# Kernel optimization log

Measured on AMD Instinct MI355X. Metric: run time of the kernel, lower is better.

Reference implementation:

```python
import jax, jax.numpy as jnp
import numpy as np

D_MODEL, D_STATE, D_CONV, EXPAND, L = 512, 16, 4, 2, 2048
D_INNER = EXPAND * D_MODEL


def _dwconv_causal(x, w, b):
    # x: (L, D), w: (D, K), b: (D,). torch Conv1d(groups=D, padding=K-1)[..., :L]
    K = w.shape[1]
    xp = jnp.pad(x, ((K - 1, 0), (0, 0)))
    windows = jnp.stack([xp[k:k + x.shape[0]] for k in range(K)], axis=-1)  # (L, D, K)
    return jnp.einsum('ldk,dk->ld', windows, w) + b


def _ssm_dir(x, inW, inb, cw, cb, xpW, xpb, dtW, dtb, outW, outb, A_log, Dp):
    xz = x @ inW + inb                      # (L, 2*Di)
    x_ssm, z = xz[:, :D_INNER], xz[:, D_INNER:]
    x_ssm = _dwconv_causal(x_ssm, cw, cb)   # (L, Di)
    sp = jax.nn.silu(x_ssm) @ xpW + xpb     # (L, Di + 2*S)
    delta = sp[:, :D_INNER]
    B = sp[:, D_INNER:D_INNER + D_STATE]
    C = sp[:, D_INNER + D_STATE:]
    dt = jax.nn.softplus(delta @ dtW + dtb)  # (L, Di)
    A = -jnp.exp(A_log)                      # (Di, S)
    dA = jnp.exp(dt[:, :, None] * A[None])                      # (L, Di, S)
    dBu = dt[:, :, None] * B[:, None, :] * x_ssm[:, :, None]    # (L, Di, S)

    def step(h, inp):
        a, bu = inp
        h = a * h + bu
        return h, h

    h0 = jnp.zeros((D_INNER, D_STATE), x.dtype)
    _, hs = jax.lax.scan(step, h0, (dA, dBu))   # (L, Di, S)
    y = jnp.einsum('lds,ls->ld', hs, C) + Dp * x_ssm
    return (y * jax.nn.silu(z)) @ outW + outb


def _make_params(key):
    ks = jax.random.split(key, 32)
    i = iter(range(32))
    def w(shape, scale=0.02):
        return (jax.random.normal(ks[next(i)], shape, jnp.float32) * scale)
    p = {}
    for pre in ('fwd_', 'bwd_'):
        p[pre + 'in_W'] = w((D_MODEL, 2 * D_INNER))
        p[pre + 'in_b'] = w((2 * D_INNER,))
        p[pre + 'conv_w'] = w((D_INNER, D_CONV), 0.1)
        p[pre + 'conv_b'] = w((D_INNER,))
        p[pre + 'xp_W'] = w((D_INNER, D_INNER + 2 * D_STATE))
        p[pre + 'xp_b'] = w((D_INNER + 2 * D_STATE,))
        p[pre + 'dt_W'] = w((D_INNER, D_INNER))
        p[pre + 'dt_b'] = w((D_INNER,))
        p[pre + 'out_W'] = w((D_INNER, D_MODEL))
        p[pre + 'out_b'] = w((D_MODEL,))
    p['A_log'] = jax.random.normal(ks[next(i)], (D_INNER, D_STATE), jnp.float32) * 0.5
    p['D_param'] = jnp.ones((D_INNER,), jnp.float32)
    p['fusion_W'] = w((2 * D_MODEL, D_MODEL))
    p['fusion_b'] = w((D_MODEL,))
    return p


def setup_inputs() -> dict:
    key = jax.random.key(0)
    kx, kp = jax.random.split(key)
    inp = {'x': jax.random.normal(kx, (L, D_MODEL), jnp.float32)}
    inp.update(_make_params(kp))
    return inp


def reference(x,
              fwd_in_W, fwd_in_b, fwd_conv_w, fwd_conv_b, fwd_xp_W, fwd_xp_b,
              fwd_dt_W, fwd_dt_b, fwd_out_W, fwd_out_b,
              bwd_in_W, bwd_in_b, bwd_conv_w, bwd_conv_b, bwd_xp_W, bwd_xp_b,
              bwd_dt_W, bwd_dt_b, bwd_out_W, bwd_out_b,
              A_log, D_param, fusion_W, fusion_b):
    out_fwd = _ssm_dir(x, fwd_in_W, fwd_in_b, fwd_conv_w, fwd_conv_b,
                       fwd_xp_W, fwd_xp_b, fwd_dt_W, fwd_dt_b,
                       fwd_out_W, fwd_out_b, A_log, D_param)
    out_bwd = _ssm_dir(x[::-1], bwd_in_W, bwd_in_b, bwd_conv_w, bwd_conv_b,
                       bwd_xp_W, bwd_xp_b, bwd_dt_W, bwd_dt_b,
                       bwd_out_W, bwd_out_b, A_log, D_param)[::-1]
    return jnp.concatenate([out_fwd, out_bwd], axis=-1) @ fusion_W + fusion_b
```

## Files before the change

kernel.cpp:

```cpp
#include <hip/hip_runtime.h>
#include <cmath>

#define L_SEQ 2048
#define DM 512
#define DI 1024
#define DS 16
#define NSP 1056
#define NC 64
#define CL 32

typedef unsigned short ushortT;
typedef unsigned int u32;
typedef __attribute__((ext_vector_type(8))) short short8;
typedef __attribute__((ext_vector_type(4))) unsigned short ushort4_t;
typedef __attribute__((ext_vector_type(4))) float float4_t;
typedef __attribute__((address_space(1))) u32 gu32;
typedef __attribute__((address_space(3))) u32 lu32;

__device__ __forceinline__ float sigm(float x) { return 1.0f / (1.0f + __expf(-x)); }

__device__ __forceinline__ ushortT f2bf(float f) {
    unsigned u = __float_as_uint(f);
    unsigned r = u + 0x7FFFu + ((u >> 16) & 1u);
    return (ushortT)(r >> 16);
}
__device__ __forceinline__ float b2f(ushortT u) {
    return __uint_as_float(((u32)u) << 16);
}
__device__ __forceinline__ void gl2lds16(const ushortT* g, ushortT* l) {
    __builtin_amdgcn_global_load_lds((gu32*)g, (lu32*)l, 16, 0, 0);
}

struct WC {
    const float* src[11];
    ushortT* dst[11];
    int ss[11], soff[11], ds_[11], tN[11], mode[11];
    int off[12];
};

struct KP {
    WC wc; int nW, nprep;
    const float* x; ushortT* XB;
    const float *xpb0, *xpb1, *dtW0, *dtW1, *dtb0, *dtb1;
    const float *outb0, *outb1, *fuW, *fub;
    float *BFdt0, *BFdt1, *BFof;
    const float *inb0, *inb1;
    ushortT *WtIn, *WtDt, *WtFu, *WtXpF, *XpD, *OutC, *WtOF2;
    ushortT *XSb, *Zb, *SCb, *DTbB, *Gb;
    float *BCf;
    const float *cw0, *cw1, *cb0, *cb1;
    const float *Alog, *Dp;
    float *Pend, *Hl, *Hs;
    float* out;
};

template<int BM, int BN>
__device__ void gemm_core(
    ushortT* As, ushortT* Bs, int bm, int bn,
    const ushortT* __restrict__ A, int lda, int revA,
    const ushortT* __restrict__ A2, int dualK,
    const ushortT* __restrict__ W,
    const float* __restrict__ bias,
    float* __restrict__ Cf, int ldcf,
    float* __restrict__ Cf2, int ldcf2, int Nsplit,
    ushortT* __restrict__ Cb, int ldcb,
    ushortT* __restrict__ Cb2, int ldcb2,
    int M, int N, int K, int epi)
{
    constexpr int BK = 64;
    constexpr int MI = BM / 32;
    constexpr int NI = BN / 32;
    constexpr int CA = BM / 32;
    constexpr int CB = BN / 32;

    const int tid  = threadIdx.x;
    const int wave = tid >> 6;
    const int lane = tid & 63;
    const int quad = lane >> 4;
    const int r    = lane & 15;
    const int wm   = (wave >> 1) * (BM / 2);
    const int wn   = (wave & 1) * (BN / 2);

    const int lrow = lane >> 3;
    const int lk   = ((lane & 7) ^ lrow) * 8;

    const ushortT* gA[CA]; const ushortT* gA2[CA]; ushortT* lA[CA];
    #pragma unroll
    for (int c = 0; c < CA; ++c) {
        int row = bm + c * 32 + wave * 8 + lrow;
        int r0 = revA ? (M - 1 - row) : row;
        gA[c] = A + (size_t)r0 * lda + lk;
        gA2[c] = dualK ? (A2 + (size_t)(M - 1 - row) * lda + lk) : gA[c];
        lA[c] = &As[(c * 32 + wave * 8) * BK];
    }
    const ushortT* gB[CB]; ushortT* lB[CB];
    #pragma unroll
    for (int c = 0; c < CB; ++c) {
        int row = bn + c * 32 + wave * 8 + lrow;
        if (row > N - 1) row = N - 1;
        gB[c] = W + (size_t)row * K + lk;
        lB[c] = &Bs[(c * 32 + wave * 8) * BK];
    }

    float4_t acc[MI][NI];
    #pragma unroll
    for (int i = 0; i < MI; ++i)
        #pragma unroll
        for (int j = 0; j < NI; ++j)
            acc[i][j] = (float4_t){0.f, 0.f, 0.f, 0.f};

    const int nsteps = K >> 6;

    auto stage = [&](int step) {
        int kq = step << 6;
        #pragma unroll
        for (int c = 0; c < CA; ++c) {
            const ushortT* s = (!dualK || kq < 1024) ? gA[c] + kq : gA2[c] + (kq - 1024);
            gl2lds16(s, lA[c]);
        }
        #pragma unroll
        for (int c = 0; c < CB; ++c)
            gl2lds16(gB[c] + kq, lB[c]);
    };
    auto compute = [&]() {
        #pragma unroll
        for (int kh = 0; kh < 2; ++kh) {
            const int slot = (((kh * 4 + quad) ^ (lane & 7)) * 8);
            short8 af[MI], bf[NI];
            #pragma unroll
            for (int mi = 0; mi < MI; ++mi)
                af[mi] = *(const short8*)&As[(wm + mi * 16 + r) * BK + slot];
            #pragma unroll
            for (int ni = 0; ni < NI; ++ni)
                bf[ni] = *(const short8*)&Bs[(wn + ni * 16 + r) * BK + slot];
            #pragma unroll
            for (int mi = 0; mi < MI; ++mi)
                #pragma unroll
                for (int ni = 0; ni < NI; ++ni)
                    acc[mi][ni] = __builtin_amdgcn_mfma_f32_16x16x32_bf16(
                        af[mi], bf[ni], acc[mi][ni], 0, 0, 0);
        }
    };

    stage(0);
    for (int i = 0; i < nsteps; ++i) {
        __syncthreads();
        compute();
        if (i + 1 < nsteps) {
            __syncthreads();
            stage(i + 1);
        }
    }

    #pragma unroll
    for (int mi = 0; mi < MI; ++mi) {
        int rowb = bm + wm + mi * 16 + quad * 4;
        #pragma unroll
        for (int ni = 0; ni < NI; ++ni) {
            int gn = bn + wn + ni * 16 + r;
            if (gn < N) {
                float bv = bias ? bias[gn] : 0.0f;
                #pragma unroll
                for (int j = 0; j < 4; ++j) {
                    int orow = rowb + j;
                    float v = acc[mi][ni][j] + bv;
                    if (gn < Nsplit) {
                        if (epi == 1) v = (v > 20.0f) ? v : log1pf(__expf(v));
                        if (Cf) Cf[(size_t)orow * ldcf + gn] = v;
                        if (Cb) Cb[(size_t)orow * ldcb + gn] = f2bf(v);
                    } else {
                        if (Cf2) Cf2[(size_t)orow * ldcf2 + gn - Nsplit] = v;
                        if (Cb2) Cb2[(size_t)orow * ldcb2 + gn - Nsplit] = f2bf(v);
                    }
                }
            }
        }
    }
}

__global__ __launch_bounds__(256) void prep_k(KP p)
{
    __shared__ ushortT smem[2624];
    ushortT (*t)[33] = (ushortT(*)[33])smem;
    float* red = (float*)(smem + 2112);
    int b = blockIdx.x;
    int tid = threadIdx.x;
    if (b < p.nW) {
        const WC& wc = p.wc;
        int m = 0;
        while (b >= wc.off[m + 1]) ++m;
        int tl = b - wc.off[m];
        int n0 = (tl % wc.tN[m]) * 32;
        int k0 = (tl / wc.tN[m]) * 32;
        const float* W = wc.src[m];
        ushortT* D = wc.dst[m];
        int ss = wc.ss[m], soff = wc.soff[m], ds = wc.ds_[m];
        int tx = tid & 31, ty = tid >> 5;
        if (wc.mode[m] == 1) {
            #pragma unroll
            for (int i = 0; i < 32; i += 8)
                D[(size_t)(k0 + ty + i) * ds + n0 + tx] =
                    f2bf(W[(size_t)(k0 + ty + i) * ss + soff + n0 + tx]);
        } else {
            #pragma unroll
            for (int i = 0; i < 32; i += 8)
                t[ty + i][tx] = f2bf(W[(size_t)(k0 + ty + i) * ss + soff + n0 + tx]);
            __syncthreads();
            #pragma unroll
            for (int i = 0; i < 32; i += 8)
                D[(size_t)(n0 + ty + i) * ds + k0 + tx] = t[tx][ty + i];
        }
        return;
    }
    b -= p.nW;
    if (b < 1024) {
        int i = (b * 256 + tid) * 4;
        float4_t v = *(const float4_t*)(p.x + i);
        p.XB[i + 0] = f2bf(v[0]); p.XB[i + 1] = f2bf(v[1]);
        p.XB[i + 2] = f2bf(v[2]); p.XB[i + 3] = f2bf(v[3]);
        return;
    }
    int o = b - 1024;
    float acc = 0.0f;
    if (o < 2112) {
        int dir = o >= 1056;
        int m = o - dir * 1056;
        const float* xpb = dir ? p.xpb1 : p.xpb0;
        float* BF = dir ? p.BFdt1 : p.BFdt0;
        if (m >= 1024) {
            if (tid == 0) BF[m] = xpb[m];
            return;
        }
        const float* dtW = dir ? p.dtW1 : p.dtW0;
        const float* dtb = dir ? p.dtb1 : p.dtb0;
        for (int n = tid; n < 1024; n += 256) acc += xpb[n] * dtW[n * 1024 + m];
        red[tid] = acc;
        __syncthreads();
        for (int s = 128; s > 0; s >>= 1) {
            if (tid < s) red[tid] += red[tid + s];
            __syncthreads();
        }
        if (tid == 0) BF[m] = red[0] + dtb[m];
    } else {
        int n = o - 2112;
        for (int j = tid; j < 1024; j += 256) {
            float ob = (j < 512) ? p.outb0[j] : p.outb1[j - 512];
            acc += ob * p.fuW[(size_t)j * 512 + n];
        }
        red[tid] = acc;
        __syncthreads();
        for (int s = 128; s > 0; s >>= 1) {
            if (tid < s) red[tid] += red[tid + s];
            __syncthreads();
        }
        if (tid == 0) p.BFof[n] = red[0] + p.fub[n];
    }
}

__global__ __launch_bounds__(256) void mega_k(KP p)
{
    __shared__ ushortT As[128 * 64];
    __shared__ ushortT Bs[64 * 64];
    int job = blockIdx.x;
    if (job < 1024) {
        int xc = job & 7;
        int k = job >> 3;
        int dir = xc & 1;
        int q = xc >> 1;
        int bx = q * 8 + (k & 7);
        int by = k >> 3;
        gemm_core<128, 64>(As, Bs, by * 128, bx * 64,
            p.XB, DM, dir, nullptr, 0,
            p.WtIn + (size_t)dir * 2 * DI * DM,
            dir ? p.inb1 : p.inb0,
            nullptr, 0, nullptr, 0, DI,
            p.XSb + (size_t)dir * L_SEQ * DI, DI,
            p.Zb + (size_t)dir * L_SEQ * DI, DI,
            L_SEQ, 2 * DI, DM, 0);
    } else if (job < 1536) {
        int j = job - 1024;
        int d = j >> 8;
        int t = j & 255;
        gemm_core<64, 64>(As, Bs, (t >> 4) * 64, (t & 15) * 64,
            p.WtDt + (size_t)d * DI * DI, DI, 0, nullptr, 0,
            p.XpD + (size_t)d * DI * DI,
            nullptr, nullptr, 0, nullptr, 0, DI,
            p.WtXpF + (size_t)d * NSP * DI, DI, nullptr, 0,
            DI, DI, DI, 0);
    } else {
        int j = job - 1536;
        int d = j >> 7;
        int t = j & 127;
        gemm_core<64, 64>(As, Bs, (t >> 4) * 64, (t & 15) * 64,
            p.WtFu + (size_t)d * DM, DI, 0, nullptr, 0,
            p.OutC + (size_t)d * DI * DM,
            nullptr, nullptr, 0, nullptr, 0, DI,
            p.WtOF2 + (size_t)d * DI, 2 * DI, nullptr, 0,
            DM, DI, DM, 0);
    }
}

__global__ __launch_bounds__(256) void conv_k(KP p)
{
    int job = blockIdx.x;
    int dir = job >> 11;
    int bx = job & 2047;
    const ushortT* XSb = p.XSb + (size_t)dir * L_SEQ * DI;
    ushortT* SCb = p.SCb + (size_t)dir * L_SEQ * DI;
    const float* cw = dir ? p.cw1 : p.cw0;
    const float* cb = dir ? p.cb1 : p.cb0;
    int idx = (bx * 256 + threadIdx.x) * 4;
    int d4 = idx & (DI - 1);
    int l = idx >> 10;
    ushort4_t r0 = *(const ushort4_t*)(XSb + (size_t)l * DI + d4);
    ushort4_t r1 = (l >= 1) ? *(const ushort4_t*)(XSb + (size_t)(l - 1) * DI + d4) : (ushort4_t){0,0,0,0};
    ushort4_t r2 = (l >= 2) ? *(const ushort4_t*)(XSb + (size_t)(l - 2) * DI + d4) : (ushort4_t){0,0,0,0};
    ushort4_t r3 = (l >= 3) ? *(const ushort4_t*)(XSb + (size_t)(l - 3) * DI + d4) : (ushort4_t){0,0,0,0};
    ushort4_t outv;
    #pragma unroll
    for (int j = 0; j < 4; ++j) {
        int d = d4 + j;
        float acc = cb[d] + cw[d * 4 + 0] * b2f(r3[j]) + cw[d * 4 + 1] * b2f(r2[j])
                  + cw[d * 4 + 2] * b2f(r1[j]) + cw[d * 4 + 3] * b2f(r0[j]);
        outv[j] = f2bf(acc * sigm(acc));
    }
    *(ushort4_t*)(SCb + idx) = outv;
}

__global__ __launch_bounds__(256) void xp_k(KP p)
{
    __shared__ ushortT As[128 * 64];
    __shared__ ushortT Bs[64 * 64];
    int job = blockIdx.x;
    int xc = job & 7;
    int k = job >> 3;
    int dir = xc & 1;
    int mq = xc >> 1;
    int bx = k >> 2;
    int by = mq * 4 + (k & 3);
    gemm_core<128, 64>(As, Bs, by * 128, bx * 64,
        p.SCb + (size_t)dir * L_SEQ * DI, DI, 0, nullptr, 0,
        p.WtXpF + (size_t)dir * NSP * DI,
        dir ? p.BFdt1 : p.BFdt0,
        nullptr, 0,
        p.BCf + (size_t)dir * L_SEQ * 32, 32, DI,
        p.DTbB + (size_t)dir * L_SEQ * DI, DI, nullptr, 0,
        L_SEQ, NSP, DI, 1);
}

__global__ __launch_bounds__(256) void scanA_k(KP p)
{
    __shared__ float Bsh[CL][DS];
    int job = blockIdx.x;
    int dir = job >> 8;
    int c = (job & 255) >> 2;
    int d = (job & 3) * 256 + threadIdx.x;
    const ushortT* DTb = p.DTbB + (size_t)dir * L_SEQ * DI;
    const ushortT* XSb = p.XSb + (size_t)dir * L_SEQ * DI;
    const float* BC = p.BCf + (size_t)dir * L_SEQ * 32;
    const float* cw = dir ? p.cw1 : p.cw0;
    const float* cb = dir ? p.cb1 : p.cb0;
    int l0 = c * CL;
    for (int i = threadIdx.x; i < CL * DS; i += 256) {
        int ll = i >> 4, ss = i & 15;
        Bsh[ll][ss] = BC[(size_t)(l0 + ll) * 32 + ss];
    }
    __syncthreads();
    float w0 = cw[d * 4 + 0], w1 = cw[d * 4 + 1], w2 = cw[d * 4 + 2], w3 = cw[d * 4 + 3];
    float cbv = cb[d];
    float x3 = (l0 >= 3) ? b2f(XSb[(size_t)(l0 - 3) * DI + d]) : 0.f;
    float x2 = (l0 >= 2) ? b2f(XSb[(size_t)(l0 - 2) * DI + d]) : 0.f;
    float x1 = (l0 >= 1) ? b2f(XSb[(size_t)(l0 - 1) * DI + d]) : 0.f;
    float Ae[DS], h[DS], P[DS];
    #pragma unroll
    for (int s = 0; s < DS; ++s) { Ae[s] = -__expf(p.Alog[d * DS + s]); h[s] = 0.f; P[s] = 1.f; }
    for (int t = 0; t < CL; ++t) {
        int l = l0 + t;
        float x0 = b2f(XSb[(size_t)l * DI + d]);
        float xv = cbv + w0 * x3 + w1 * x2 + w2 * x1 + w3 * x0;
        x3 = x2; x2 = x1; x1 = x0;
        float dt = b2f(DTb[(size_t)l * DI + d]);
        float dtx = dt * xv;
        #pragma unroll
        for (int s = 0; s < DS; ++s) {
            float e = __expf(dt * Ae[s]);
            h[s] = e * h[s] + dtx * Bsh[t][s];
            P[s] *= e;
        }
    }
    size_t o = ((size_t)(dir * NC + c) * DI + d) * DS;
    #pragma unroll
    for (int s = 0; s < DS; ++s) { p.Pend[o + s] = P[s]; p.Hl[o + s] = h[s]; }
}

__global__ __launch_bounds__(256) void scanB_k(KP p)
{
    int idx = blockIdx.x * 256 + threadIdx.x;
    float h = 0.f;
    int ds = idx & 16383;
    int dir = idx >> 14;
    for (int c = 0; c < NC; ++c) {
        size_t o = ((size_t)(dir * NC + c)) * (DI * DS) + ds;
        p.Hs[o] = h;
        h = p.Pend[o] * h + p.Hl[o];
    }
}

__global__ __launch_bounds__(256) void scanC_k(KP p)
{
    __shared__ float Bsh[CL][DS];
    __shared__ float Csh[CL][DS];
    int job = blockIdx.x;
    int dir = job >> 8;
    int c = (job & 255) >> 2;
    int d = (job & 3) * 256 + threadIdx.x;
    const ushortT* DTb = p.DTbB + (size_t)dir * L_SEQ * DI;
    const ushortT* XSb = p.XSb + (size_t)dir * L_SEQ * DI;
    const float* BC = p.BCf + (size_t)dir * L_SEQ * 32;
    const ushortT* Zb = p.Zb + (size_t)dir * L_SEQ * DI;
    ushortT* Gb = p.Gb + (size_t)dir * L_SEQ * DI;
    const float* cw = dir ? p.cw1 : p.cw0;
    const float* cb = dir ? p.cb1 : p.cb0;
    int l0 = c * CL;
    for (int i = threadIdx.x; i < CL * DS; i += 256) {
        int ll = i >> 4, ss = i & 15;
        size_t base = (size_t)(l0 + ll) * 32;
        Bsh[ll][ss] = BC[base + ss];
        Csh[ll][ss] = BC[base + DS + ss];
    }
    __syncthreads();
    float w0 = cw[d * 4 + 0], w1 = cw[d * 4 + 1], w2 = cw[d * 4 + 2], w3 = cw[d * 4 + 3];
    float cbv = cb[d];
    float x3 = (l0 >= 3) ? b2f(XSb[(size_t)(l0 - 3) * DI + d]) : 0.f;
    float x2 = (l0 >= 2) ? b2f(XSb[(size_t)(l0 - 2) * DI + d]) : 0.f;
    float x1 = (l0 >= 1) ? b2f(XSb[(size_t)(l0 - 1) * DI + d]) : 0.f;
    float Ae[DS], h[DS];
    size_t o = ((size_t)(dir * NC + c) * DI + d) * DS;
    #pragma unroll
    for (int s = 0; s < DS; ++s) { Ae[s] = -__expf(p.Alog[d * DS + s]); h[s] = p.Hs[o + s]; }
    float dpv = p.Dp[d];
    for (int t = 0; t < CL; ++t) {
        int l = l0 + t;
        float x0 = b2f(XSb[(size_t)l * DI + d]);
        float xv = cbv + w0 * x3 + w1 * x2 + w2 * x1 + w3 * x0;
        x3 = x2; x2 = x1; x1 = x0;
        float dt = b2f(DTb[(size_t)l * DI + d]);
        float dtx = dt * xv;
        float y = 0.f;
        #pragma unroll
        for (int s = 0; s < DS; ++s) {
            float e = __expf(dt * Ae[s]);
            h[s] = e * h[s] + dtx * Bsh[t][s];
            y += h[s] * Csh[t][s];
        }
        y += dpv * xv;
        float z = b2f(Zb[(size_t)l * DI + d]);
        Gb[(size_t)l * DI + d] = f2bf(y * (z * sigm(z)));
    }
}

__global__ __launch_bounds__(256) void final_k(KP p)
{
    __shared__ ushortT As[64 * 64];
    __shared__ ushortT Bs[32 * 64];
    int job = blockIdx.x;
    int xc = job & 7;
    int k = job >> 3;
    int by = xc * 4 + (k & 3);
    int bx = k >> 2;
    gemm_core<64, 32>(As, Bs, by * 64, bx * 32,
        p.Gb, DI, 0, p.Gb + (size_t)L_SEQ * DI, 1,
        p.WtOF2, p.BFof,
        p.out, DM, nullptr, 0, DM,
        nullptr, 0, nullptr, 0,
        L_SEQ, DM, 2 * DI, 0);
}

extern "C" void kernel_launch(void* const* d_in, const int* in_sizes, int n_in,
                              void* d_out, int out_size, void* d_ws, size_t ws_size,
                              hipStream_t stream)
{
    (void)in_sizes; (void)n_in; (void)out_size; (void)ws_size;
    const float* x = (const float*)d_in[0];
    const float* inW[2]  = {(const float*)d_in[1],  (const float*)d_in[11]};
    const float* inb[2]  = {(const float*)d_in[2],  (const float*)d_in[12]};
    const float* cw[2]   = {(const float*)d_in[3],  (const float*)d_in[13]};
    const float* cb[2]   = {(const float*)d_in[4],  (const float*)d_in[14]};
    const float* xpW[2]  = {(const float*)d_in[5],  (const float*)d_in[15]};
    const float* xpb[2]  = {(const float*)d_in[6],  (const float*)d_in[16]};
    const float* dtW[2]  = {(const float*)d_in[7],  (const float*)d_in[17]};
    const float* dtb[2]  = {(const float*)d_in[8],  (const float*)d_in[18]};
    const float* outW[2] = {(const float*)d_in[9],  (const float*)d_in[19]};
    const float* outb[2] = {(const float*)d_in[10], (const float*)d_in[20]};
    const float* Alog = (const float*)d_in[21];
    const float* Dp   = (const float*)d_in[22];
    const float* fuW  = (const float*)d_in[23];
    const float* fub  = (const float*)d_in[24];
    float* out = (float*)d_out;

    float* ws = (float*)d_ws;
    size_t off = 0;
    auto alloc = [&](size_t n) { float* p = ws + off; off += n; return p; };
    float* BCf  = alloc((size_t)2 * L_SEQ * 32);
    float* Pend = alloc((size_t)2 * NC * DI * DS);
    float* Hl   = alloc((size_t)2 * NC * DI * DS);
    float* Hs   = alloc((size_t)2 * NC * DI * DS);
    float* BFdt0 = alloc(1056);
    float* BFdt1 = alloc(1056);
    float* BFof  = alloc(512);

    ushortT* wsu = (ushortT*)(ws + off);
    size_t uoff = 0;
    auto ualloc = [&](size_t n) { ushortT* p = wsu + uoff; uoff += n; return p; };
    ushortT* WtIn  = ualloc((size_t)2 * (2 * DI) * DM);
    ushortT* WtDt  = ualloc((size_t)2 * DI * DI);
    ushortT* WtFu  = ualloc((size_t)DM * DI);
    ushortT* WtXpF = ualloc((size_t)2 * NSP * DI);
    ushortT* XpD   = ualloc((size_t)2 * DI * DI);
    ushortT* OutC  = ualloc((size_t)2 * DI * DM);
    ushortT* WtOF2 = ualloc((size_t)DM * 2 * DI);
    ushortT* XB    = ualloc((size_t)L_SEQ * DM);
    ushortT* XSb   = ualloc((size_t)2 * L_SEQ * DI);
    ushortT* Zb    = ualloc((size_t)2 * L_SEQ * DI);
    ushortT* SCb   = ualloc((size_t)2 * L_SEQ * DI);
    ushortT* DTbB  = ualloc((size_t)2 * L_SEQ * DI);
    ushortT* Gb    = ualloc((size_t)2 * L_SEQ * DI);

    KP p;
    struct E { const float* s; ushortT* d; int ss, so, ds, N, K, mode; };
    E es[11] = {
        {inW[0],  WtIn,                          2 * DI, 0,    DM, 2 * DI, DM, 0},
        {inW[1],  WtIn + (size_t)2 * DI * DM,    2 * DI, 0,    DM, 2 * DI, DM, 0},
        {dtW[0],  WtDt,                          DI,     0,    DI, DI,     DI, 0},
        {dtW[1],  WtDt + (size_t)DI * DI,        DI,     0,    DI, DI,     DI, 0},
        {fuW,     WtFu,                          DM,     0,    DI, DM,     DI, 0},
        {xpW[0],  WtXpF + (size_t)DI * DI,       NSP,    DI,   DI, 32,     DI, 0},
        {xpW[1],  WtXpF + (size_t)NSP * DI + (size_t)DI * DI, NSP, DI, DI, 32, DI, 0},
        {xpW[0],  XpD,                           NSP,    0,    DI, DI,     DI, 1},
        {xpW[1],  XpD + (size_t)DI * DI,         NSP,    0,    DI, DI,     DI, 1},
        {outW[0], OutC,                          DM,     0,    DM, DM,     DI, 1},
        {outW[1], OutC + (size_t)DI * DM,        DM,     0,    DM, DM,     DI, 1},
    };
    p.wc.off[0] = 0;
    for (int m = 0; m < 11; ++m) {
        p.wc.src[m] = es[m].s; p.wc.dst[m] = es[m].d;
        p.wc.ss[m] = es[m].ss; p.wc.soff[m] = es[m].so; p.wc.ds_[m] = es[m].ds;
        p.wc.tN[m] = es[m].N / 32; p.wc.mode[m] = es[m].mode;
        p.wc.off[m + 1] = p.wc.off[m] + (es[m].N / 32) * (es[m].K / 32);
    }
    p.nW = p.wc.off[11];
    p.nprep = p.nW + 1024 + 2624;
    p.x = x; p.XB = XB;
    p.xpb0 = xpb[0]; p.xpb1 = xpb[1];
    p.dtW0 = dtW[0]; p.dtW1 = dtW[1];
    p.dtb0 = dtb[0]; p.dtb1 = dtb[1];
    p.outb0 = outb[0]; p.outb1 = outb[1];
    p.fuW = fuW; p.fub = fub;
    p.BFdt0 = BFdt0; p.BFdt1 = BFdt1; p.BFof = BFof;
    p.inb0 = inb[0]; p.inb1 = inb[1];
    p.WtIn = WtIn; p.WtDt = WtDt; p.WtFu = WtFu; p.WtXpF = WtXpF;
    p.XpD = XpD; p.OutC = OutC; p.WtOF2 = WtOF2;
    p.XSb = XSb; p.Zb = Zb; p.SCb = SCb; p.DTbB = DTbB; p.Gb = Gb;
    p.BCf = BCf;
    p.cw0 = cw[0]; p.cw1 = cw[1]; p.cb0 = cb[0]; p.cb1 = cb[1];
    p.Alog = Alog; p.Dp = Dp;
    p.Pend = Pend; p.Hl = Hl; p.Hs = Hs;
    p.out = out;

    dim3 blk(256);
    prep_k <<<dim3(p.nprep), blk, 0, stream>>>(p);
    mega_k <<<dim3(1792),    blk, 0, stream>>>(p);
    conv_k <<<dim3(4096),    blk, 0, stream>>>(p);
    xp_k   <<<dim3(544),     blk, 0, stream>>>(p);
    scanA_k<<<dim3(512),     blk, 0, stream>>>(p);
    scanB_k<<<dim3(128),     blk, 0, stream>>>(p);
    scanC_k<<<dim3(512),     blk, 0, stream>>>(p);
    final_k<<<dim3(512),     blk, 0, stream>>>(p);
}
```

Before: 341.1 us.

## Double-buffer GEMM LDS tiles and fuse three-pass scan into one flag-synchronized kernel

The GEMM core now ping-pongs between two LDS buffers so the load of the next K-tile overlaps the MFMA work on the current one, which also cuts the barriers per step. The three scan kernels (chunk-local scan, carry propagation, final scan) become a single kernel. Each chunk block publishes its end state and decay product with a release flag, then waits on all earlier chunks' flags and combines their states itself. This removes two launches and the Hs round trip, but makes LDS per block twice as large and relies on the 512 blocks all being resident at once to avoid a spin-wait deadlock. Each chunk also does O(c) redundant combine work.

```diff
diff --git a/kernel.cpp b/kernel.cpp
--- a/kernel.cpp
+++ b/kernel.cpp
@@ -50,7 +50,8 @@
     float *BCf;
     const float *cw0, *cw1, *cb0, *cb1;
     const float *Alog, *Dp;
-    float *Pend, *Hl, *Hs;
+    float *Pend, *Hl;
+    int* flags;
     float* out;
 };
 
@@ -72,6 +73,8 @@
     constexpr int NI = BN / 32;
     constexpr int CA = BM / 32;
     constexpr int CB = BN / 32;
+    constexpr int ABUF = BM * BK;
+    constexpr int BBUF = BN * BK;
 
     const int tid  = threadIdx.x;
     const int wave = tid >> 6;
@@ -111,28 +114,28 @@
 
     const int nsteps = K >> 6;
 
-    auto stage = [&](int step) {
+    auto stage = [&](int step, int buf) {
         int kq = step << 6;
         #pragma unroll
         for (int c = 0; c < CA; ++c) {
             const ushortT* s = (!dualK || kq < 1024) ? gA[c] + kq : gA2[c] + (kq - 1024);
-            gl2lds16(s, lA[c]);
+            gl2lds16(s, lA[c] + buf * ABUF);
         }
         #pragma unroll
         for (int c = 0; c < CB; ++c)
-            gl2lds16(gB[c] + kq, lB[c]);
+            gl2lds16(gB[c] + kq, lB[c] + buf * BBUF);
     };
-    auto compute = [&]() {
+    auto compute = [&](int buf) {
         #pragma unroll
         for (int kh = 0; kh < 2; ++kh) {
             const int slot = (((kh * 4 + quad) ^ (lane & 7)) * 8);
             short8 af[MI], bf[NI];
             #pragma unroll
             for (int mi = 0; mi < MI; ++mi)
-                af[mi] = *(const short8*)&As[(wm + mi * 16 + r) * BK + slot];
+                af[mi] = *(const short8*)&As[buf * ABUF + (wm + mi * 16 + r) * BK + slot];
             #pragma unroll
             for (int ni = 0; ni < NI; ++ni)
-                bf[ni] = *(const short8*)&Bs[(wn + ni * 16 + r) * BK + slot];
+                bf[ni] = *(const short8*)&Bs[buf * BBUF + (wn + ni * 16 + r) * BK + slot];
             #pragma unroll
             for (int mi = 0; mi < MI; ++mi)
                 #pragma unroll
@@ -142,14 +145,14 @@
         }
     };
 
-    stage(0);
-    for (int i = 0; i < nsteps; ++i) {
+    stage(0, 0);
+    for (int i = 0; i < nsteps; i += 2) {
         __syncthreads();
-        compute();
-        if (i + 1 < nsteps) {
-            __syncthreads();
-            stage(i + 1);
-        }
+        if (i + 1 < nsteps) stage(i + 1, 1);
+        compute(0);
+        __syncthreads();
+        if (i + 2 < nsteps) stage(i + 2, 0);
+        compute(1);
     }
 
     #pragma unroll
@@ -259,8 +262,8 @@
 
 __global__ __launch_bounds__(256) void mega_k(KP p)
 {
-    __shared__ ushortT As[128 * 64];
-    __shared__ ushortT Bs[64 * 64];
+    __shared__ ushortT As[2 * 128 * 64];
+    __shared__ ushortT Bs[2 * 64 * 64];
     int job = blockIdx.x;
     if (job < 1024) {
         int xc = job & 7;
@@ -329,8 +332,8 @@
 
 __global__ __launch_bounds__(256) void xp_k(KP p)
 {
-    __shared__ ushortT As[128 * 64];
-    __shared__ ushortT Bs[64 * 64];
+    __shared__ ushortT As[2 * 128 * 64];
+    __shared__ ushortT Bs[2 * 64 * 64];
     int job = blockIdx.x;
     int xc = job & 7;
     int k = job >> 3;
@@ -348,72 +351,15 @@
         L_SEQ, NSP, DI, 1);
 }
 
-__global__ __launch_bounds__(256) void scanA_k(KP p)
-{
-    __shared__ float Bsh[CL][DS];
-    int job = blockIdx.x;
-    int dir = job >> 8;
-    int c = (job & 255) >> 2;
-    int d = (job & 3) * 256 + threadIdx.x;
-    const ushortT* DTb = p.DTbB + (size_t)dir * L_SEQ * DI;
-    const ushortT* XSb = p.XSb + (size_t)dir * L_SEQ * DI;
-    const float* BC = p.BCf + (size_t)dir * L_SEQ * 32;
-    const float* cw = dir ? p.cw1 : p.cw0;
-    const float* cb = dir ? p.cb1 : p.cb0;
-    int l0 = c * CL;
-    for (int i = threadIdx.x; i < CL * DS; i += 256) {
-        int ll = i >> 4, ss = i & 15;
-        Bsh[ll][ss] = BC[(size_t)(l0 + ll) * 32 + ss];
-    }
-    __syncthreads();
-    float w0 = cw[d * 4 + 0], w1 = cw[d * 4 + 1], w2 = cw[d * 4 + 2], w3 = cw[d * 4 + 3];
-    float cbv = cb[d];
-    float x3 = (l0 >= 3) ? b2f(XSb[(size_t)(l0 - 3) * DI + d]) : 0.f;
-    float x2 = (l0 >= 2) ? b2f(XSb[(size_t)(l0 - 2) * DI + d]) : 0.f;
-    float x1 = (l0 >= 1) ? b2f(XSb[(size_t)(l0 - 1) * DI + d]) : 0.f;
-    float Ae[DS], h[DS], P[DS];
-    #pragma unroll
-    for (int s = 0; s < DS; ++s) { Ae[s] = -__expf(p.Alog[d * DS + s]); h[s] = 0.f; P[s] = 1.f; }
-    for (int t = 0; t < CL; ++t) {
-        int l = l0 + t;
-        float x0 = b2f(XSb[(size_t)l * DI + d]);
-        float xv = cbv + w0 * x3 + w1 * x2 + w2 * x1 + w3 * x0;
-        x3 = x2; x2 = x1; x1 = x0;
-        float dt = b2f(DTb[(size_t)l * DI + d]);
-        float dtx = dt * xv;
-        #pragma unroll
-        for (int s = 0; s < DS; ++s) {
-            float e = __expf(dt * Ae[s]);
-            h[s] = e * h[s] + dtx * Bsh[t][s];
-            P[s] *= e;
-        }
-    }
-    size_t o = ((size_t)(dir * NC + c) * DI + d) * DS;
-    #pragma unroll
-    for (int s = 0; s < DS; ++s) { p.Pend[o + s] = P[s]; p.Hl[o + s] = h[s]; }
-}
-
-__global__ __launch_bounds__(256) void scanB_k(KP p)
-{
-    int idx = blockIdx.x * 256 + threadIdx.x;
-    float h = 0.f;
-    int ds = idx & 16383;
-    int dir = idx >> 14;
-    for (int c = 0; c < NC; ++c) {
-        size_t o = ((size_t)(dir * NC + c)) * (DI * DS) + ds;
-        p.Hs[o] = h;
-        h = p.Pend[o] * h + p.Hl[o];
-    }
-}
-
-__global__ __launch_bounds__(256) void scanC_k(KP p)
+__global__ __launch_bounds__(256) void scan_k(KP p)
 {
     __shared__ float Bsh[CL][DS];
     __shared__ float Csh[CL][DS];
     int job = blockIdx.x;
     int dir = job >> 8;
-    int c = (job & 255) >> 2;
-    int d = (job & 3) * 256 + threadIdx.x;
+    int c = (job >> 2) & 63;
+    int dblk = job & 3;
+    int d = dblk * 256 + threadIdx.x;
     const ushortT* DTb = p.DTbB + (size_t)dir * L_SEQ * DI;
     const ushortT* XSb = p.XSb + (size_t)dir * L_SEQ * DI;
     const float* BC = p.BCf + (size_t)dir * L_SEQ * 32;
@@ -421,7 +367,9 @@
     ushortT* Gb = p.Gb + (size_t)dir * L_SEQ * DI;
     const float* cw = dir ? p.cw1 : p.cw0;
     const float* cb = dir ? p.cb1 : p.cb0;
+    const int fb = (dir * 4 + dblk) * NC;
     int l0 = c * CL;
+
     for (int i = threadIdx.x; i < CL * DS; i += 256) {
         int ll = i >> 4, ss = i & 15;
         size_t base = (size_t)(l0 + ll) * 32;
@@ -429,40 +377,93 @@
         Csh[ll][ss] = BC[base + DS + ss];
     }
     __syncthreads();
+
     float w0 = cw[d * 4 + 0], w1 = cw[d * 4 + 1], w2 = cw[d * 4 + 2], w3 = cw[d * 4 + 3];
     float cbv = cb[d];
-    float x3 = (l0 >= 3) ? b2f(XSb[(size_t)(l0 - 3) * DI + d]) : 0.f;
-    float x2 = (l0 >= 2) ? b2f(XSb[(size_t)(l0 - 2) * DI + d]) : 0.f;
-    float x1 = (l0 >= 1) ? b2f(XSb[(size_t)(l0 - 1) * DI + d]) : 0.f;
-    float Ae[DS], h[DS];
-    size_t o = ((size_t)(dir * NC + c) * DI + d) * DS;
-    #pragma unroll
-    for (int s = 0; s < DS; ++s) { Ae[s] = -__expf(p.Alog[d * DS + s]); h[s] = p.Hs[o + s]; }
-    float dpv = p.Dp[d];
-    for (int t = 0; t < CL; ++t) {
-        int l = l0 + t;
-        float x0 = b2f(XSb[(size_t)l * DI + d]);
-        float xv = cbv + w0 * x3 + w1 * x2 + w2 * x1 + w3 * x0;
-        x3 = x2; x2 = x1; x1 = x0;
-        float dt = b2f(DTb[(size_t)l * DI + d]);
-        float dtx = dt * xv;
-        float y = 0.f;
+    float Ae[DS];
+    #pragma unroll
+    for (int s = 0; s < DS; ++s) Ae[s] = -__expf(p.Alog[d * DS + s]);
+
+    {
+        float x3 = (l0 >= 3) ? b2f(XSb[(size_t)(l0 - 3) * DI + d]) : 0.f;
+        float x2 = (l0 >= 2) ? b2f(XSb[(size_t)(l0 - 2) * DI + d]) : 0.f;
+        float x1 = (l0 >= 1) ? b2f(XSb[(size_t)(l0 - 1) * DI + d]) : 0.f;
+        float h[DS], P[DS];
+        #pragma unroll
+        for (int s = 0; s < DS; ++s) { h[s] = 0.f; P[s] = 1.f; }
+        for (int t = 0; t < CL; ++t) {
+            int l = l0 + t;
+            float x0 = b2f(XSb[(size_t)l * DI + d]);
+            float xv = cbv + w0 * x3 + w1 * x2 + w2 * x1 + w3 * x0;
+            x3 = x2; x2 = x1; x1 = x0;
+            float dt = b2f(DTb[(size_t)l * DI + d]);
+            float dtx = dt * xv;
+            #pragma unroll
+            for (int s = 0; s < DS; ++s) {
+                float e = __expf(dt * Ae[s]);
+                h[s] = e * h[s] + dtx * Bsh[t][s];
+                P[s] *= e;
+            }
+        }
+        size_t o = ((size_t)(dir * NC + c) * DI + d) * DS;
+        #pragma unroll
+        for (int s = 0; s < DS; ++s) { p.Pend[o + s] = P[s]; p.Hl[o + s] = h[s]; }
+    }
+    __syncthreads();
+    __threadfence();
+    if (threadIdx.x == 0)
+        __hip_atomic_store(&p.flags[fb + c], 1, __ATOMIC_RELEASE, __HIP_MEMORY_SCOPE_AGENT);
+
+    if (threadIdx.x == 0) {
+        for (int j = 0; j < c; ++j)
+            while (__hip_atomic_load(&p.flags[fb + j], __ATOMIC_ACQUIRE,
+                                     __HIP_MEMORY_SCOPE_AGENT) == 0)
+                __builtin_amdgcn_s_sleep(8);
+    }
+    __syncthreads();
+    float h[DS];
+    #pragma unroll
+    for (int s = 0; s < DS; ++s) h[s] = 0.f;
+    for (int j = 0; j < c; ++j) {
+        size_t o = ((size_t)(dir * NC + j) * DI + d) * DS;
         #pragma unroll
         for (int s = 0; s < DS; ++s) {
-            float e = __expf(dt * Ae[s]);
-            h[s] = e * h[s] + dtx * Bsh[t][s];
-            y += h[s] * Csh[t][s];
-        }
-        y += dpv * xv;
-        float z = b2f(Zb[(size_t)l * DI + d]);
-        Gb[(size_t)l * DI + d] = f2bf(y * (z * sigm(z)));
+            float P = __hip_atomic_load(&p.Pend[o + s], __ATOMIC_RELAXED, __HIP_MEMORY_SCOPE_AGENT);
+            float H = __hip_atomic_load(&p.Hl[o + s],   __ATOMIC_RELAXED, __HIP_MEMORY_SCOPE_AGENT);
+            h[s] = P * h[s] + H;
+        }
+    }
+
+    {
+        float x3 = (l0 >= 3) ? b2f(XSb[(size_t)(l0 - 3) * DI + d]) : 0.f;
+        float x2 = (l0 >= 2) ? b2f(XSb[(size_t)(l0 - 2) * DI + d]) : 0.f;
+        float x1 = (l0 >= 1) ? b2f(XSb[(size_t)(l0 - 1) * DI + d]) : 0.f;
+        float dpv = p.Dp[d];
+        for (int t = 0; t < CL; ++t) {
+            int l = l0 + t;
+            float x0 = b2f(XSb[(size_t)l * DI + d]);
+            float xv = cbv + w0 * x3 + w1 * x2 + w2 * x1 + w3 * x0;
+            x3 = x2; x2 = x1; x1 = x0;
+            float dt = b2f(DTb[(size_t)l * DI + d]);
+            float dtx = dt * xv;
+            float y = 0.f;
+            #pragma unroll
+            for (int s = 0; s < DS; ++s) {
+                float e = __expf(dt * Ae[s]);
+                h[s] = e * h[s] + dtx * Bsh[t][s];
+                y += h[s] * Csh[t][s];
+            }
+            y += dpv * xv;
+            float z = b2f(Zb[(size_t)l * DI + d]);
+            Gb[(size_t)l * DI + d] = f2bf(y * (z * sigm(z)));
+        }
     }
 }
 
 __global__ __launch_bounds__(256) void final_k(KP p)
 {
-    __shared__ ushortT As[64 * 64];
-    __shared__ ushortT Bs[32 * 64];
+    __shared__ ushortT As[2 * 64 * 64];
+    __shared__ ushortT Bs[2 * 32 * 64];
     int job = blockIdx.x;
     int xc = job & 7;
     int k = job >> 3;
@@ -504,10 +505,10 @@
     float* BCf  = alloc((size_t)2 * L_SEQ * 32);
     float* Pend = alloc((size_t)2 * NC * DI * DS);
     float* Hl   = alloc((size_t)2 * NC * DI * DS);
-    float* Hs   = alloc((size_t)2 * NC * DI * DS);
     float* BFdt0 = alloc(1056);
     float* BFdt1 = alloc(1056);
     float* BFof  = alloc(512);
+    int*   flags = (int*)alloc(512);
 
     ushortT* wsu = (ushortT*)(ws + off);
     size_t uoff = 0;
@@ -564,16 +565,16 @@
     p.BCf = BCf;
     p.cw0 = cw[0]; p.cw1 = cw[1]; p.cb0 = cb[0]; p.cb1 = cb[1];
     p.Alog = Alog; p.Dp = Dp;
-    p.Pend = Pend; p.Hl = Hl; p.Hs = Hs;
+    p.Pend = Pend; p.Hl = Hl;
+    p.flags = flags;
     p.out = out;
 
     dim3 blk(256);
+    hipMemsetAsync(flags, 0, 512 * sizeof(int), stream);
     prep_k <<<dim3(p.nprep), blk, 0, stream>>>(p);
     mega_k <<<dim3(1792),    blk, 0, stream>>>(p);
     conv_k <<<dim3(4096),    blk, 0, stream>>>(p);
     xp_k   <<<dim3(544),     blk, 0, stream>>>(p);
-    scanA_k<<<dim3(512),     blk, 0, stream>>>(p);
-    scanB_k<<<dim3(128),     blk, 0, stream>>>(p);
-    scanC_k<<<dim3(512),     blk, 0, stream>>>(p);
+    scan_k <<<dim3(512),     blk, 0, stream>>>(p);
     final_k<<<dim3(512),     blk, 0, stream>>>(p);
 }
```

Measured after the change: 952.7 us. 179% more time.

## Double-buffer LDS in gemm_core and split final GEMM over directions with atomics

Applied to the files above, without the earlier changes.

The shared GEMM core now uses two LDS buffers and processes two K-steps per loop iteration. Each buffer is filled by asynchronous global-to-LDS loads while the other is being computed on, which drops one barrier per K-step and overlaps load latency with MFMA work. The final output GEMM is split across the two directions into twice as many blocks, accumulating into a zeroed output with float atomicAdd. That split needs an extra memset launch and makes the summation order nondeterministic. Doubling LDS per block (up to 48KB in mega_k/xp_k) can lower occupancy.

```diff
diff --git a/kernel.cpp b/kernel.cpp
--- a/kernel.cpp
+++ b/kernel.cpp
@@ -58,8 +58,7 @@
 __device__ void gemm_core(
     ushortT* As, ushortT* Bs, int bm, int bn,
     const ushortT* __restrict__ A, int lda, int revA,
-    const ushortT* __restrict__ A2, int dualK,
-    const ushortT* __restrict__ W,
+    const ushortT* __restrict__ W, int ldw,
     const float* __restrict__ bias,
     float* __restrict__ Cf, int ldcf,
     float* __restrict__ Cf2, int ldcf2, int Nsplit,
@@ -72,6 +71,8 @@
     constexpr int NI = BN / 32;
     constexpr int CA = BM / 32;
     constexpr int CB = BN / 32;
+    constexpr int ABUF = BM * BK;
+    constexpr int BBUF = BN * BK;
 
     const int tid  = threadIdx.x;
     const int wave = tid >> 6;
@@ -84,13 +85,12 @@
     const int lrow = lane >> 3;
     const int lk   = ((lane & 7) ^ lrow) * 8;
 
-    const ushortT* gA[CA]; const ushortT* gA2[CA]; ushortT* lA[CA];
+    const ushortT* gA[CA]; ushortT* lA[CA];
     #pragma unroll
     for (int c = 0; c < CA; ++c) {
         int row = bm + c * 32 + wave * 8 + lrow;
         int r0 = revA ? (M - 1 - row) : row;
         gA[c] = A + (size_t)r0 * lda + lk;
-        gA2[c] = dualK ? (A2 + (size_t)(M - 1 - row) * lda + lk) : gA[c];
         lA[c] = &As[(c * 32 + wave * 8) * BK];
     }
     const ushortT* gB[CB]; ushortT* lB[CB];
@@ -98,7 +98,7 @@
     for (int c = 0; c < CB; ++c) {
         int row = bn + c * 32 + wave * 8 + lrow;
         if (row > N - 1) row = N - 1;
-        gB[c] = W + (size_t)row * K + lk;
+        gB[c] = W + (size_t)row * ldw + lk;
         lB[c] = &Bs[(c * 32 + wave * 8) * BK];
     }
 
@@ -111,28 +111,24 @@
 
     const int nsteps = K >> 6;
 
-    auto stage = [&](int step) {
+    auto stage = [&](int step, int buf) {
         int kq = step << 6;
         #pragma unroll
-        for (int c = 0; c < CA; ++c) {
-            const ushortT* s = (!dualK || kq < 1024) ? gA[c] + kq : gA2[c] + (kq - 1024);
-            gl2lds16(s, lA[c]);
-        }
-        #pragma unroll
-        for (int c = 0; c < CB; ++c)
-            gl2lds16(gB[c] + kq, lB[c]);
+        for (int c = 0; c < CA; ++c) gl2lds16(gA[c] + kq, lA[c] + buf * ABUF);
+        #pragma unroll
+        for (int c = 0; c < CB; ++c) gl2lds16(gB[c] + kq, lB[c] + buf * BBUF);
     };
-    auto compute = [&]() {
+    auto compute = [&](int buf) {
         #pragma unroll
         for (int kh = 0; kh < 2; ++kh) {
             const int slot = (((kh * 4 + quad) ^ (lane & 7)) * 8);
             short8 af[MI], bf[NI];
             #pragma unroll
             for (int mi = 0; mi < MI; ++mi)
-                af[mi] = *(const short8*)&As[(wm + mi * 16 + r) * BK + slot];
+                af[mi] = *(const short8*)&As[buf * ABUF + (wm + mi * 16 + r) * BK + slot];
             #pragma unroll
             for (int ni = 0; ni < NI; ++ni)
-                bf[ni] = *(const short8*)&Bs[(wn + ni * 16 + r) * BK + slot];
+                bf[ni] = *(const short8*)&Bs[buf * BBUF + (wn + ni * 16 + r) * BK + slot];
             #pragma unroll
             for (int mi = 0; mi < MI; ++mi)
                 #pragma unroll
@@ -142,14 +138,14 @@
         }
     };
 
-    stage(0);
-    for (int i = 0; i < nsteps; ++i) {
+    stage(0, 0);
+    for (int i = 0; i < nsteps; i += 2) {
         __syncthreads();
-        compute();
-        if (i + 1 < nsteps) {
-            __syncthreads();
-            stage(i + 1);
-        }
+        if (i + 1 < nsteps) stage(i + 1, 1);
+        compute(0);
+        __syncthreads();
+        if (i + 2 < nsteps) stage(i + 2, 0);
+        compute(1);
     }
 
     #pragma unroll
@@ -164,7 +160,9 @@
                 for (int j = 0; j < 4; ++j) {
                     int orow = rowb + j;
                     float v = acc[mi][ni][j] + bv;
-                    if (gn < Nsplit) {
+                    if (epi == 3) {
+                        atomicAdd(&Cf[(size_t)orow * ldcf + gn], v);
+                    } else if (gn < Nsplit) {
                         if (epi == 1) v = (v > 20.0f) ? v : log1pf(__expf(v));
                         if (Cf) Cf[(size_t)orow * ldcf + gn] = v;
                         if (Cb) Cb[(size_t)orow * ldcb + gn] = f2bf(v);
@@ -259,8 +257,8 @@
 
 __global__ __launch_bounds__(256) void mega_k(KP p)
 {
-    __shared__ ushortT As[128 * 64];
-    __shared__ ushortT Bs[64 * 64];
+    __shared__ ushortT As[2 * 128 * 64];
+    __shared__ ushortT Bs[2 * 64 * 64];
     int job = blockIdx.x;
     if (job < 1024) {
         int xc = job & 7;
@@ -270,8 +268,8 @@
         int bx = q * 8 + (k & 7);
         int by = k >> 3;
         gemm_core<128, 64>(As, Bs, by * 128, bx * 64,
-            p.XB, DM, dir, nullptr, 0,
-            p.WtIn + (size_t)dir * 2 * DI * DM,
+            p.XB, DM, dir,
+            p.WtIn + (size_t)dir * 2 * DI * DM, DM,
             dir ? p.inb1 : p.inb0,
             nullptr, 0, nullptr, 0, DI,
             p.XSb + (size_t)dir * L_SEQ * DI, DI,
@@ -282,8 +280,8 @@
         int d = j >> 8;
         int t = j & 255;
         gemm_core<64, 64>(As, Bs, (t >> 4) * 64, (t & 15) * 64,
-            p.WtDt + (size_t)d * DI * DI, DI, 0, nullptr, 0,
-            p.XpD + (size_t)d * DI * DI,
+            p.WtDt + (size_t)d * DI * DI, DI, 0,
+            p.XpD + (size_t)d * DI * DI, DI,
             nullptr, nullptr, 0, nullptr, 0, DI,
             p.WtXpF + (size_t)d * NSP * DI, DI, nullptr, 0,
             DI, DI, DI, 0);
@@ -292,8 +290,8 @@
         int d = j >> 7;
         int t = j & 127;
         gemm_core<64, 64>(As, Bs, (t >> 4) * 64, (t & 15) * 64,
-            p.WtFu + (size_t)d * DM, DI, 0, nullptr, 0,
-            p.OutC + (size_t)d * DI * DM,
+            p.WtFu + (size_t)d * DM, DI, 0,
+            p.OutC + (size_t)d * DI * DM, DM,
             nullptr, nullptr, 0, nullptr, 0, DI,
             p.WtOF2 + (size_t)d * DI, 2 * DI, nullptr, 0,
             DM, DI, DM, 0);
@@ -329,8 +327,8 @@
 
 __global__ __launch_bounds__(256) void xp_k(KP p)
 {
-    __shared__ ushortT As[128 * 64];
-    __shared__ ushortT Bs[64 * 64];
+    __shared__ ushortT As[2 * 128 * 64];
+    __shared__ ushortT Bs[2 * 64 * 64];
     int job = blockIdx.x;
     int xc = job & 7;
     int k = job >> 3;
@@ -339,8 +337,8 @@
     int bx = k >> 2;
     int by = mq * 4 + (k & 3);
     gemm_core<128, 64>(As, Bs, by * 128, bx * 64,
-        p.SCb + (size_t)dir * L_SEQ * DI, DI, 0, nullptr, 0,
-        p.WtXpF + (size_t)dir * NSP * DI,
+        p.SCb + (size_t)dir * L_SEQ * DI, DI, 0,
+        p.WtXpF + (size_t)dir * NSP * DI, DI,
         dir ? p.BFdt1 : p.BFdt0,
         nullptr, 0,
         p.BCf + (size_t)dir * L_SEQ * 32, 32, DI,
@@ -461,19 +459,22 @@
 
 __global__ __launch_bounds__(256) void final_k(KP p)
 {
-    __shared__ ushortT As[64 * 64];
-    __shared__ ushortT Bs[32 * 64];
+    __shared__ ushortT As[2 * 64 * 64];
+    __shared__ ushortT Bs[2 * 32 * 64];
     int job = blockIdx.x;
-    int xc = job & 7;
-    int k = job >> 3;
+    int dir = job & 1;
+    int t = job >> 1;
+    int xc = t & 7;
+    int k = t >> 3;
     int by = xc * 4 + (k & 3);
     int bx = k >> 2;
     gemm_core<64, 32>(As, Bs, by * 64, bx * 32,
-        p.Gb, DI, 0, p.Gb + (size_t)L_SEQ * DI, 1,
-        p.WtOF2, p.BFof,
+        p.Gb + (size_t)dir * L_SEQ * DI, DI, dir,
+        p.WtOF2 + (size_t)dir * DI, 2 * DI,
+        dir ? nullptr : p.BFof,
         p.out, DM, nullptr, 0, DM,
         nullptr, 0, nullptr, 0,
-        L_SEQ, DM, 2 * DI, 0);
+        L_SEQ, DM, DI, 3);
 }
 
 extern "C" void kernel_launch(void* const* d_in, const int* in_sizes, int n_in,
@@ -568,6 +569,7 @@
     p.out = out;
 
     dim3 blk(256);
+    hipMemsetAsync(out, 0, (size_t)L_SEQ * DM * sizeof(float), stream);
     prep_k <<<dim3(p.nprep), blk, 0, stream>>>(p);
     mega_k <<<dim3(1792),    blk, 0, stream>>>(p);
     conv_k <<<dim3(4096),    blk, 0, stream>>>(p);
@@ -575,5 +577,5 @@
     scanA_k<<<dim3(512),     blk, 0, stream>>>(p);
     scanB_k<<<dim3(128),     blk, 0, stream>>>(p);
     scanC_k<<<dim3(512),     blk, 0, stream>>>(p);
-    final_k<<<dim3(512),     blk, 0, stream>>>(p);
-}
+    final_k<<<dim3(1024),    blk, 0, stream>>>(p);
+}
```

Measured after the change: 339.0 us. Within noise of the previous version (-0.6%).
